# Kernel optimization log

Measured on AMD Instinct MI355X. Metric: run time of the kernel, lower is better.

## Reference

```python
import jax, jax.numpy as jnp
import numpy as np
import math

D_MODEL = 1024
D_STATE = 64
D_CONV = 4
EXPAND = 2
D_INNER = EXPAND * D_MODEL
DT_RANK = max(16, D_MODEL // 16)
SEQ_LEN = 2048
BATCH = 4

def setup_inputs() -> dict:
    key = jax.random.key(0)
    ks = jax.random.split(key, 16)
    s = lambda *sh: 1.0 / math.sqrt(sh[-1])
    x = jax.random.normal(ks[0], (SEQ_LEN, BATCH, D_MODEL), jnp.float32)
    state = jnp.zeros((BATCH, D_INNER, D_STATE), jnp.float32)
    W_in = jax.random.normal(ks[1], (2 * D_INNER, D_MODEL), jnp.float32) * s(2 * D_INNER, D_MODEL)
    b_in = jnp.zeros((2 * D_INNER,), jnp.float32)
    conv_w = jax.random.normal(ks[2], (D_INNER, 1, D_CONV), jnp.float32) * s(1, D_CONV)
    conv_b = jnp.zeros((D_INNER,), jnp.float32)
    W_xp = jax.random.normal(ks[3], (DT_RANK + 2 * D_STATE, D_INNER), jnp.float32) * s(1, D_INNER)
    b_xp = jnp.zeros((DT_RANK + 2 * D_STATE,), jnp.float32)
    W_dt = jax.random.normal(ks[4], (D_INNER, DT_RANK), jnp.float32) * s(1, DT_RANK)
    # dt bias init as in module: softplus-inverse of dt in [1e-3, 0.1]
    dt = jnp.exp(jax.random.uniform(ks[5], (D_INNER,)) * (math.log(0.1) - math.log(0.001)) + math.log(0.001))
    b_dt = dt + jnp.log(-jnp.expm1(-dt))
    A_log = jnp.log(jnp.broadcast_to(jnp.arange(1, D_STATE + 1, dtype=jnp.float32)[None, :], (D_INNER, D_STATE)))
    D = jnp.ones((D_INNER,), jnp.float32)
    W_out = jax.random.normal(ks[6], (D_MODEL, D_INNER), jnp.float32) * s(1, D_INNER)
    b_out = jnp.zeros((D_MODEL,), jnp.float32)
    ln_g = jnp.ones((D_MODEL,), jnp.float32)
    ln_b = jnp.zeros((D_MODEL,), jnp.float32)
    return dict(x=x, state=state, W_in=W_in, b_in=b_in, conv_w=conv_w, conv_b=conv_b,
                W_xp=W_xp, b_xp=b_xp, W_dt=W_dt, b_dt=b_dt, A_log=A_log, D=D,
                W_out=W_out, b_out=b_out, ln_g=ln_g, ln_b=ln_b)

def _silu(v):
    return v * jax.nn.sigmoid(v)

def _forward(x, state, W_in, b_in, conv_w, conv_b, W_xp, b_xp, W_dt, b_dt, A_log, D, W_out, b_out, ln_g, ln_b):
    S, B, _ = x.shape
    xz = x @ W_in.T + b_in                      # [S,B,2*di]
    x_inner, z = jnp.split(xz, 2, axis=-1)      # [S,B,di] each
    # causal depthwise conv1d: pad left (d_conv-1), matching conv1d(pad=K-1)[..., :S]
    xc = jnp.transpose(x_inner, (1, 2, 0))      # [B,di,S]
    xc = jax.lax.conv_general_dilated(
        xc, conv_w, window_strides=(1,), padding=[(D_CONV - 1, 0)],
        dimension_numbers=('NCH', 'OIH', 'NCH'), feature_group_count=D_INNER)
    xc = xc + conv_b[None, :, None]
    x_conv = _silu(jnp.transpose(xc, (2, 0, 1)))  # [S,B,di]
    # input-dependent projections over full sequence
    xp = x_conv @ W_xp.T + b_xp                 # [S,B,dt_rank+2*ds]
    dt_low, B_seq, C_seq = jnp.split(xp, [DT_RANK, DT_RANK + D_STATE], axis=-1)
    # NOTE: original adds dt_proj.bias twice (Linear already includes it)
    dt = jax.nn.softplus(dt_low @ W_dt.T + 2.0 * b_dt)  # [S,B,di]
    A = -jnp.exp(A_log)                         # [di,ds]

    def step(carry, inp):
        dt_t, B_t, C_t, x_t = inp               # [B,di],[B,ds],[B,ds],[B,di]
        dA = jnp.exp(dt_t[..., None] * A)       # [B,di,ds]
        dBx = (dt_t * x_t)[..., None] * B_t[:, None, :]  # [B,di,ds]
        new = carry * dA + dBx
        y = jnp.einsum('bdn,bn->bd', new, C_t) + D * x_t
        return new, y

    final_state, ys = jax.lax.scan(step, state, (dt, B_seq, C_seq, x_conv))
    ys = ys * _silu(z)                          # [S,B,di]
    out = jnp.mean(ys, axis=0) @ W_out.T + b_out  # [B,d_model]
    mu = jnp.mean(out, axis=-1, keepdims=True)
    var = jnp.var(out, axis=-1, keepdims=True)
    out = (out - mu) / jnp.sqrt(var + 1e-5) * ln_g + ln_b
    return out, final_state

def reference(x, state, W_in, b_in, conv_w, conv_b, W_xp, b_xp, W_dt, b_dt, A_log, D, W_out, b_out, ln_g, ln_b):
    return _forward(x, state, W_in, b_in, conv_w, conv_b, W_xp, b_xp, W_dt, b_dt, A_log, D, W_out, b_out, ln_g, ln_b)
```

## Files before the change

### kernel.cpp

```cpp
#include <hip/hip_runtime.h>
#include <hip/hip_fp16.h>

typedef __attribute__((ext_vector_type(8))) short short8;
typedef __attribute__((ext_vector_type(8))) unsigned short u16x8;
typedef __attribute__((ext_vector_type(4))) float f32x4;

#define S_LEN 2048
#define BATCH 4
#define DM 1024
#define DI 2048
#define DS 64
#define DTR 64
#define XPW 192
#define NCH 16
#define CLEN 128

typedef const __attribute__((address_space(4))) unsigned* cu_as4;

__device__ __forceinline__ unsigned short f2bf(float f){
  unsigned u = __builtin_bit_cast(unsigned, f);
  u += 0x7fffu + ((u >> 16) & 1u);
  return (unsigned short)(u >> 16);
}
__device__ __forceinline__ float bf2f(unsigned short h){
  unsigned u = ((unsigned)h) << 16;
  return __builtin_bit_cast(float, u);
}
__device__ __forceinline__ void gload16(const void* g, void* l){
  __builtin_amdgcn_global_load_lds((const __attribute__((address_space(1))) void*)g,
                                   (__attribute__((address_space(3))) void*)l, 16, 0, 0);
}
__device__ __forceinline__ float siluf_(float v){ return v / (1.f + __expf(-v)); }

__global__ __launch_bounds__(256) void cvt_all_k(const float* __restrict__ i0, unsigned short* __restrict__ o0,
                                                 const float* __restrict__ i1, unsigned short* __restrict__ o1,
                                                 const float* __restrict__ i2, unsigned short* __restrict__ o2,
                                                 const float* __restrict__ i3, unsigned short* __restrict__ o3)
{
  int bid = blockIdx.x;
  const float* in; unsigned short* out; int base;
  if (bid < 8192)       { in = i0; out = o0; base = bid; }
  else if (bid < 12288) { in = i1; out = o1; base = bid - 8192; }
  else if (bid < 12672) { in = i2; out = o2; base = bid - 12288; }
  else                  { in = i3; out = o3; base = bid - 12672; }
  int i = (base * 256 + threadIdx.x) * 4;
  float4 v = *(const float4*)(in + i);
  ushort4 o;
  o.x = f2bf(v.x); o.y = f2bf(v.y); o.z = f2bf(v.z); o.w = f2bf(v.w);
  *(ushort4*)(out + i) = o;
}

template<int EPI>
__global__ __launch_bounds__(256)
void gemm_bt(const unsigned short* __restrict__ A, const unsigned short* __restrict__ B,
             const float* __restrict__ bias,
             int N, int K, int lda, int ldb,
             void* __restrict__ vp0, void* __restrict__ vp1,
             const void* __restrict__ vp2, const void* __restrict__ vp3,
             int nsilu, float* __restrict__ sdt)
{
  __shared__ unsigned short As[128 * 32];
  __shared__ unsigned short Bs[128 * 32];
  const int tid  = threadIdx.x;
  const int lane = tid & 63;
  const int wid  = tid >> 6;
  int bm, bn;
  if constexpr (EPI == 2) {
    int flat = blockIdx.y * 64 + blockIdx.x;
    int swz = (flat & 7) * 256 + (flat >> 3);
    bm = swz & 63; bn = swz >> 6;
  } else {
    bm = blockIdx.x; bn = blockIdx.y;
  }
  int k_lo = 0, k_hi = K;
  if constexpr (EPI == 3) { k_lo = blockIdx.z * 512; k_hi = k_lo + 512; }
  const int r0 = tid >> 2;
  const int c0 = (tid & 3) * 8;
  int brow0 = bn * 128 + r0;        if (brow0 > N - 1) brow0 = N - 1;
  int brow1 = bn * 128 + 64 + r0;   if (brow1 > N - 1) brow1 = N - 1;
  const unsigned short* pa0 = A + (size_t)(bm * 128 + r0) * lda + c0;
  const unsigned short* pa1 = A + (size_t)(bm * 128 + 64 + r0) * lda + c0;
  const unsigned short* pb0 = B + (size_t)brow0 * ldb + c0;
  const unsigned short* pb1 = B + (size_t)brow1 * ldb + c0;
  f32x4 acc[4][4] = {};
  const int fr = lane & 15, fq = lane >> 4;
  const int wm = (wid >> 1) * 64, wn = (wid & 1) * 64;
  const int aoff0 = (wm + fr) * 32 + fq * 8;
  const int boff0 = (wn + fr) * 32 + fq * 8;
  for (int k0 = k_lo; k0 < k_hi; k0 += 32) {
    __syncthreads();
    gload16(pa0 + k0, &As[tid * 8]);
    gload16(pa1 + k0, &As[2048 + tid * 8]);
    gload16(pb0 + k0, &Bs[tid * 8]);
    gload16(pb1 + k0, &Bs[2048 + tid * 8]);
    __syncthreads();
    short8 av[4], bv[4];
#pragma unroll
    for (int i = 0; i < 4; i++) av[i] = *(const short8*)&As[aoff0 + i * 16 * 32];
#pragma unroll
    for (int i = 0; i < 4; i++) bv[i] = *(const short8*)&Bs[boff0 + i * 16 * 32];
#pragma unroll
    for (int i = 0; i < 4; i++)
#pragma unroll
      for (int j = 0; j < 4; j++)
        acc[i][j] = __builtin_amdgcn_mfma_f32_16x16x32_bf16(av[i], bv[j], acc[i][j], 0, 0, 0);
  }

  if constexpr (EPI == 3) {
    float* xpp = (float*)vp0;
    const size_t kb = (size_t)blockIdx.z * 8192 * 256;
#pragma unroll
    for (int i = 0; i < 4; i++) {
#pragma unroll
      for (int j = 0; j < 4; j++) {
        int gc = bn * 128 + wn + j * 16 + fr;
#pragma unroll
        for (int e = 0; e < 4; e++) {
          int gr = bm * 128 + wm + i * 16 + fq * 4 + e;
          xpp[kb + (size_t)gr * 256 + gc] = acc[i][j][e];
        }
      }
    }
  } else if constexpr (EPI == 2) {
    unsigned short* xib = (unsigned short*)vp0;
    unsigned short* grm = (unsigned short*)vp1;
#pragma unroll
    for (int i = 0; i < 4; i++) {
#pragma unroll
      for (int j = 0; j < 4; j++) {
        int gc = bn * 128 + wn + j * 16 + fr;
        float bb = bias[gc];
#pragma unroll
        for (int e = 0; e < 4; e++) {
          int gr = bm * 128 + wm + i * 16 + fq * 4 + e;
          float v = acc[i][j][e] + bb;
          if (gc < nsilu) xib[(size_t)gr * DI + gc] = f2bf(v);
          else            grm[(size_t)gr * DI + (gc - nsilu)] = f2bf(siluf_(v));
        }
      }
    }
  } else {
    unsigned* dtH = (unsigned*)vp0;
    unsigned* dxg = (unsigned*)vp1;
    const unsigned short* xcb = (const unsigned short*)vp2;
    const unsigned short* grm = (const unsigned short*)vp3;
#pragma unroll
    for (int j = 0; j < 4; j++) {
      int gc = bn * 128 + wn + j * 16 + fr;
      float bb2 = 2.f * bias[gc];
#pragma unroll
      for (int i = 0; i < 4; i++)
#pragma unroll
        for (int e = 0; e < 4; e++) {
          float v = acc[i][j][e] + bb2;
          acc[i][j][e] = fmaxf(v, 0.f) + log1pf(__expf(-fabsf(v)));
        }
    }
    __shared__ unsigned short hbuf[256 * 36];
    const int myc = wn >> 6;
    const int tbase = wm / 4;
    const int chk = bm >> 2;
    for (int cc = 0; cc < 2; ++cc) {
      __syncthreads();
      if (myc == cc) {
#pragma unroll
        for (int i = 0; i < 4; i++)
#pragma unroll
          for (int j = 0; j < 4; j++) {
            int dl = j * 16 + fr;
            int t_ = tbase + i * 4 + fq;
#pragma unroll
            for (int e = 0; e < 4; e++)
              hbuf[(e * 64 + dl) * 36 + t_] = f2bf(acc[i][j][e]);
          }
      }
      __syncthreads();
#pragma unroll
      for (int k = 0; k < 4; ++k) {
        int gidx = tid + k * 256;
        int t   = gidx & 31;
        int gl8 = (gidx >> 5) & 7;
        int e   = gidx >> 8;
        int R   = e * 64 + gl8 * 8;
        uint4 o;
        o.x = (unsigned)hbuf[(R+0)*36 + t] | ((unsigned)hbuf[(R+1)*36 + t] << 16);
        o.y = (unsigned)hbuf[(R+2)*36 + t] | ((unsigned)hbuf[(R+3)*36 + t] << 16);
        o.z = (unsigned)hbuf[(R+4)*36 + t] | ((unsigned)hbuf[(R+5)*36 + t] << 16);
        o.w = (unsigned)hbuf[(R+6)*36 + t] | ((unsigned)hbuf[(R+7)*36 + t] << 16);
        size_t G = (size_t)(bn * 16 + cc * 8 + gl8);
        *(uint4*)&dtH[(((size_t)e * 256 + G) * 2048 + bm * 32 + t) * 4] = o;
      }
#pragma unroll
      for (int k = 0; k < 4; ++k) {
        int gidx = tid + k * 256;
        int t   = gidx & 31;
        int gl8 = (gidx >> 5) & 7;
        int e   = gidx >> 8;
        int gr  = (bm * 32 + t) * 4 + e;
        int col = bn * 128 + cc * 64 + gl8 * 8;
        u16x8 xv = *(const u16x8*)&xcb[(size_t)gr * DI + col];
        u16x8 gv = *(const u16x8*)&grm[(size_t)gr * DI + col];
        int R = e * 64 + gl8 * 8;
        unsigned ow[8];
#pragma unroll
        for (int u = 0; u < 8; ++u) {
          float dt = bf2f(hbuf[(R + u) * 36 + t]);
          float dtx = dt * bf2f((unsigned short)xv[u]);
          ow[u] = ((unsigned)f2bf(dtx) << 16) | (unsigned)(unsigned short)gv[u];
        }
        size_t G = (size_t)(bn * 16 + cc * 8 + gl8);
        unsigned* dst = &dxg[(((size_t)e * 256 + G) * 2048 + bm * 32 + t) * 8];
        uint4 o0, o1;
        o0.x = ow[0]; o0.y = ow[1]; o0.z = ow[2]; o0.w = ow[3];
        o1.x = ow[4]; o1.y = ow[5]; o1.z = ow[6]; o1.w = ow[7];
        *(uint4*)dst = o0;
        *(uint4*)(dst + 4) = o1;
      }
      {
        int e  = tid >> 6;
        int dl = tid & 63;
        float s = 0.f;
#pragma unroll
        for (int t = 0; t < 32; ++t)
          s += bf2f(hbuf[(e * 64 + dl) * 36 + t]);
        int g8 = bn * 16 + cc * 8 + (dl >> 3);
        atomicAdd(&sdt[(((size_t)e * NCH + chk) * 256 + g8) * 8 + (dl & 7)], s);
      }
    }
  }
}

__global__ __launch_bounds__(192) void xpred_k(const float* __restrict__ xpp,
                                               const float* __restrict__ bias,
                                               unsigned short* __restrict__ xpb,
                                               float* __restrict__ bcI)
{
  const int gr = blockIdx.x;
  const int gc = threadIdx.x;
  const size_t o = (size_t)gr * 256 + gc;
  float v = xpp[o] + xpp[o + 2097152] + xpp[o + 2 * 2097152] + xpp[o + 3 * 2097152] + bias[gc];
  xpb[(size_t)gr * XPW + gc] = f2bf(v);
  if (gc >= 64 && gc < 128)      bcI[((size_t)gr * 64 + gc - 64) * 2 + 0] = v;
  else if (gc >= 128)            bcI[((size_t)gr * 64 + gc - 128) * 2 + 1] = v;
}

__global__ __launch_bounds__(256) void convsxg_k(const unsigned short* __restrict__ xib,
                                                 const unsigned short* __restrict__ grm,
                                                 const float* __restrict__ cw,
                                                 const float* __restrict__ cb,
                                                 unsigned short* __restrict__ xcb,
                                                 float* __restrict__ sxg)
{
  const int d4 = blockIdx.x * 1024 + threadIdx.x * 4;
  const int b  = blockIdx.y;
  const int t0 = blockIdx.z * 16;
  float4 cwv[4]; float cbv[4];
#pragma unroll
  for (int j = 0; j < 4; ++j) { cwv[j] = *(const float4*)&cw[(d4 + j) * 4]; cbv[j] = cb[d4 + j]; }
  ushort4 z4; z4.x = z4.y = z4.z = z4.w = 0;
  ushort4 xm1 = (t0 >= 1) ? *(const ushort4*)&xib[((size_t)((t0 - 1) * 4 + b)) * DI + d4] : z4;
  ushort4 xm2 = (t0 >= 2) ? *(const ushort4*)&xib[((size_t)((t0 - 2) * 4 + b)) * DI + d4] : z4;
  ushort4 xm3 = (t0 >= 3) ? *(const ushort4*)&xib[((size_t)((t0 - 3) * 4 + b)) * DI + d4] : z4;
  float sa[4] = {0.f, 0.f, 0.f, 0.f};
  for (int tt = 0; tt < 16; ++tt) {
    const int t = t0 + tt;
    const size_t row = ((size_t)(t * 4 + b)) * DI + d4;
    ushort4 x0 = *(const ushort4*)&xib[row];
    ushort4 gv = *(const ushort4*)&grm[row];
    unsigned short xr[4] = {x0.x, x0.y, x0.z, x0.w};
    unsigned short r1[4] = {xm1.x, xm1.y, xm1.z, xm1.w};
    unsigned short r2[4] = {xm2.x, xm2.y, xm2.z, xm2.w};
    unsigned short r3[4] = {xm3.x, xm3.y, xm3.z, xm3.w};
    unsigned short gg[4] = {gv.x, gv.y, gv.z, gv.w};
    unsigned short ov[4];
#pragma unroll
    for (int j = 0; j < 4; ++j) {
      float s = cbv[j];
      s = fmaf(cwv[j].w, bf2f(xr[j]), s);
      s = fmaf(cwv[j].z, bf2f(r1[j]), s);
      s = fmaf(cwv[j].y, bf2f(r2[j]), s);
      s = fmaf(cwv[j].x, bf2f(r3[j]), s);
      ov[j] = f2bf(siluf_(s));
      sa[j] = fmaf(bf2f(ov[j]), bf2f(gg[j]), sa[j]);
    }
    ushort4 o; o.x = ov[0]; o.y = ov[1]; o.z = ov[2]; o.w = ov[3];
    *(ushort4*)&xcb[row] = o;
    xm3 = xm2; xm2 = xm1; xm1 = x0;
  }
#pragma unroll
  for (int j = 0; j < 4; ++j) atomicAdd(&sxg[b * DI + d4 + j], sa[j]);
}

__global__ __launch_bounds__(256) void scan_k(const unsigned* __restrict__ dtHg,
                                              const unsigned* __restrict__ dxgg,
                                              const float* __restrict__ bcI,
                                              const float* __restrict__ A_log,
                                              float* __restrict__ Pb,
                                              float* __restrict__ Fb,
                                              float* __restrict__ accp)
{
  const int tid  = threadIdx.x;
  const int lane = tid & 63;
  const int gw = __builtin_amdgcn_readfirstlane(blockIdx.x * 4 + (tid >> 6));
  const int b  = gw >> 12;
  const int c  = (gw >> 8) & 15;
  const int g  = gw & 255;
  const int d0 = g * 8;
  const float LOG2E = 1.4426950408889634f;
  float a2[8], st[8], Dr[8], Fr[8], acc[8];
#pragma unroll
  for (int j = 0; j < 8; ++j) {
    a2[j] = -__expf(A_log[(size_t)(d0 + j) * DS + lane]) * LOG2E;
    st[j] = 0.f; Dr[j] = 1.f; Fr[j] = 0.f; acc[j] = 0.f;
  }
  cu_as4 pdt = (cu_as4)(unsigned long long)(dtHg + (((size_t)(b * 256 + g)) * S_LEN + c * CLEN) * 4);
  cu_as4 pdx = (cu_as4)(unsigned long long)(dxgg + (((size_t)(b * 256 + g)) * S_LEN + c * CLEN) * 8);
  const float* pbc = bcI + (((size_t)(c * CLEN) * 4 + b) * 64 + lane) * 2;
#pragma unroll 4
  for (int t = 0; t < CLEN; ++t) {
    unsigned dw0 = pdt[t * 4 + 0], dw1 = pdt[t * 4 + 1];
    unsigned dw2 = pdt[t * 4 + 2], dw3 = pdt[t * 4 + 3];
    unsigned xs[8];
#pragma unroll
    for (int j = 0; j < 8; ++j) xs[j] = pdx[t * 8 + j];
    float2 bc = *(const float2*)(pbc + (size_t)t * 512);
    float dts[8];
    dts[0] = __builtin_bit_cast(float, dw0 << 16);
    dts[1] = __builtin_bit_cast(float, dw0 & 0xffff0000u);
    dts[2] = __builtin_bit_cast(float, dw1 << 16);
    dts[3] = __builtin_bit_cast(float, dw1 & 0xffff0000u);
    dts[4] = __builtin_bit_cast(float, dw2 << 16);
    dts[5] = __builtin_bit_cast(float, dw2 & 0xffff0000u);
    dts[6] = __builtin_bit_cast(float, dw3 << 16);
    dts[7] = __builtin_bit_cast(float, dw3 & 0xffff0000u);
#pragma unroll
    for (int j = 0; j < 8; ++j) {
      float dxs = __builtin_bit_cast(float, xs[j] & 0xffff0000u);
      float gsv = __builtin_bit_cast(float, xs[j] << 16);
      float dA = __builtin_amdgcn_exp2f(dts[j] * a2[j]);
      st[j] = fmaf(st[j], dA, dxs * bc.x);
      Dr[j] *= dA;
      float w = gsv * bc.y;
      acc[j] = fmaf(st[j], w, acc[j]);
      Fr[j] = fmaf(Dr[j], w, Fr[j]);
    }
  }
  const size_t sb = (((size_t)((b * NCH + c) * 256 + g)) * 8) * 64 + lane;
#pragma unroll
  for (int j = 0; j < 8; ++j) {
    Pb[sb + j * 64] = st[j];
    Fb[sb + j * 64] = Fr[j];
  }
#pragma unroll
  for (int j = 0; j < 8; ++j)
#pragma unroll
    for (int m = 32; m; m >>= 1) acc[j] += __shfl_xor(acc[j], m, 64);
  if (lane == 0) {
#pragma unroll
    for (int j = 0; j < 8; ++j)
      accp[(b * NCH + c) * DI + d0 + j] = acc[j];
  }
}

__global__ __launch_bounds__(256) void fixup_k(const float* __restrict__ Pb,
                                               const float* __restrict__ Fb,
                                               const float* __restrict__ sdt,
                                               const float* __restrict__ accp,
                                               const float* __restrict__ A_log,
                                               const float* __restrict__ state_in,
                                               float* __restrict__ accbuf,
                                               float* __restrict__ state_out)
{
  const int tid  = threadIdx.x;
  const int lane = tid & 63;
  const int gw = blockIdx.x * 4 + (tid >> 6);
  const int b  = gw >> 8;
  const int g  = gw & 255;
  const int d0 = g * 8;
  const float LOG2E = 1.4426950408889634f;
  float a2[8], S[8], v[8];
#pragma unroll
  for (int j = 0; j < 8; ++j) {
    a2[j] = -__expf(A_log[(size_t)(d0 + j) * DS + lane]) * LOG2E;
    S[j] = state_in[((size_t)(b * DI + d0 + j)) * DS + lane];
    v[j] = 0.f;
  }
#pragma unroll
  for (int c = 0; c < NCH; ++c) {
    const size_t sb = (((size_t)((b * NCH + c) * 256 + g)) * 8) * 64 + lane;
    const size_t se = (((size_t)(b * NCH + c)) * 256 + g) * 8;
#pragma unroll
    for (int j = 0; j < 8; ++j) {
      float P = Pb[sb + j * 64], F = Fb[sb + j * 64];
      float E = __builtin_amdgcn_exp2f(a2[j] * sdt[se + j]);
      v[j] = fmaf(F, S[j], v[j]);
      S[j] = fmaf(E, S[j], P);
    }
  }
#pragma unroll
  for (int j = 0; j < 8; ++j)
    state_out[((size_t)(b * DI + d0 + j)) * DS + lane] = S[j];
#pragma unroll
  for (int j = 0; j < 8; ++j)
#pragma unroll
    for (int m = 32; m; m >>= 1) v[j] += __shfl_xor(v[j], m, 64);
  if (lane == 0) {
#pragma unroll
    for (int j = 0; j < 8; ++j) {
      float s = v[j];
#pragma unroll
      for (int c = 0; c < NCH; ++c) s += accp[(b * NCH + c) * DI + d0 + j];
      accbuf[b * DI + d0 + j] = s;
    }
  }
}

__global__ __launch_bounds__(256) void out_gemm_k(const float* __restrict__ accb,
                                                  const float* __restrict__ sxg,
                                                  const float* __restrict__ Dv,
                                                  const float* __restrict__ W_out,
                                                  const float* __restrict__ b_out,
                                                  float* __restrict__ outpre)
{
  int b = blockIdx.y;
  int m = blockIdx.x * 8 + (threadIdx.x >> 5);
  int dl = threadIdx.x & 31;
  const float* wr = W_out + (size_t)m * DI;
  const float* ac = accb + b * DI;
  const float* sx = sxg + b * DI;
  float p = 0.f;
  for (int dd = dl; dd < DI; dd += 32) {
    float av = fmaf(Dv[dd], sx[dd], ac[dd]);
    p = fmaf(wr[dd], av, p);
  }
#pragma unroll
  for (int s = 16; s; s >>= 1) p += __shfl_xor(p, s, 32);
  if (dl == 0) outpre[b * DM + m] = p * (1.f / 2048.f) + b_out[m];
}

__global__ __launch_bounds__(256) void ln_k(const float* __restrict__ outpre,
                                            const float* __restrict__ g,
                                            const float* __restrict__ bta,
                                            float* __restrict__ dout)
{
  int b = blockIdx.x;
  const float* row = outpre + b * DM;
  float s = 0.f, s2 = 0.f, vv[4];
#pragma unroll
  for (int i = 0; i < 4; i++) {
    float v = row[threadIdx.x + i * 256];
    vv[i] = v; s += v; s2 += v * v;
  }
#pragma unroll
  for (int m = 32; m; m >>= 1) { s += __shfl_xor(s, m, 64); s2 += __shfl_xor(s2, m, 64); }
  __shared__ float rs[4], rs2[4];
  int w = threadIdx.x >> 6;
  if ((threadIdx.x & 63) == 0) { rs[w] = s; rs2[w] = s2; }
  __syncthreads();
  float S = rs[0] + rs[1] + rs[2] + rs[3];
  float S2 = rs2[0] + rs2[1] + rs2[2] + rs2[3];
  float mu = S * (1.f / 1024.f);
  float var = S2 * (1.f / 1024.f) - mu * mu;
  float inv = rsqrtf(var + 1e-5f);
#pragma unroll
  for (int i = 0; i < 4; i++) {
    int c = threadIdx.x + i * 256;
    dout[b * DM + c] = (vv[i] - mu) * inv * g[c] + bta[c];
  }
}

extern "C" void kernel_launch(void* const* d_in, const int* in_sizes, int n_in,
                              void* d_out, int out_size, void* d_ws, size_t ws_size,
                              hipStream_t stream)
{
  const float* x      = (const float*)d_in[0];
  const float* state0 = (const float*)d_in[1];
  const float* W_in   = (const float*)d_in[2];
  const float* b_in   = (const float*)d_in[3];
  const float* conv_w = (const float*)d_in[4];
  const float* conv_b = (const float*)d_in[5];
  const float* W_xp   = (const float*)d_in[6];
  const float* b_xp   = (const float*)d_in[7];
  const float* W_dt   = (const float*)d_in[8];
  const float* b_dt   = (const float*)d_in[9];
  const float* A_log  = (const float*)d_in[10];
  const float* Dvec   = (const float*)d_in[11];
  const float* W_out  = (const float*)d_in[12];
  const float* b_out  = (const float*)d_in[13];
  const float* ln_g   = (const float*)d_in[14];
  const float* ln_b   = (const float*)d_in[15];
  float* out = (float*)d_out;

  const size_t MB = 1024 * 1024;
  char* ws = (char*)d_ws;
  unsigned short* grm  = (unsigned short*)(ws + 0);
  unsigned short* xcb  = (unsigned short*)(ws + 32  * MB);
  unsigned short* xib  = (unsigned short*)(ws + 64  * MB);
  unsigned*       dtH  = (unsigned*)(ws + 64  * MB);
  unsigned short* xb   = (unsigned short*)(ws + 96  * MB);
  unsigned short* wbin = (unsigned short*)(ws + 112 * MB);
  float*          xpp  = (float*)(ws + 96 * MB);
  unsigned*       dxg  = (unsigned*)(ws + 96  * MB);
  unsigned short* xpb  = (unsigned short*)(ws + 160 * MB);
  float*          bcI  = (float*)(ws + 163 * MB);
  unsigned short* wbxp = (unsigned short*)(ws + 167 * MB);
  unsigned short* wbdt = (unsigned short*)(ws + 167 * MB + 786432);
  float*          sxg    = (float*)(ws + 168 * MB);
  float*          sdt    = (float*)(ws + 168 * MB + 32768);
  float*          accb   = (float*)(ws + 168 * MB + 557056);
  float*          outpre = (float*)(ws + 168 * MB + 589824);
  float*          accp   = (float*)(ws + 168 * MB + 606208);
  float*          Pb   = (float*)(ws + 0);
  float*          Fb   = (float*)(ws + 32 * MB);

  cvt_all_k<<<12800, 256, 0, stream>>>(x, xb, W_in, wbin, W_xp, wbxp, W_dt, wbdt);
  hipMemsetAsync(sxg, 0, 557056, stream);
  gemm_bt<2><<<dim3(64, 32), 256, 0, stream>>>(xb, wbin, b_in, 4096, 1024, 1024, 1024,
                                               xib, grm, nullptr, nullptr, 2048, nullptr);
  convsxg_k<<<dim3(2, 4, 128), 256, 0, stream>>>(xib, grm, conv_w, conv_b, xcb, sxg);
  gemm_bt<3><<<dim3(64, 2, 4), 256, 0, stream>>>(xcb, wbxp, nullptr, 192, 2048, 2048, 2048,
                                                 xpp, nullptr, nullptr, nullptr, 0, nullptr);
  xpred_k<<<8192, 192, 0, stream>>>(xpp, b_xp, xpb, bcI);
  gemm_bt<1><<<dim3(64, 16), 256, 0, stream>>>(xpb, wbdt, b_dt, 2048, 64, XPW, 64,
                                               dtH, dxg, xcb, grm, 0, sdt);
  scan_k<<<4096, 256, 0, stream>>>(dtH, dxg, bcI, A_log, Pb, Fb, accp);
  fixup_k<<<256, 256, 0, stream>>>(Pb, Fb, sdt, accp, A_log, state0, accb, out + 4096);
  out_gemm_k<<<dim3(128, 4), 256, 0, stream>>>(accb, sxg, Dvec, W_out, b_out, outpre);
  ln_k<<<4, 256, 0, stream>>>(outpre, ln_g, ln_b, out);
}
```

Measured before the change: 487.3 us.

## Add dedicated multi-stage pipelined input-projection GEMM kernel

Replaces the generic gemm_bt<2> input projection with a specialized kernel that keeps four LDS stages and issues global-to-LDS loads three tiles ahead, using explicit vmcnt waits and one barrier per k-step. It also uses a swizzled LDS layout for bank-conflict avoidance, splits MFMA groups with interleaved loads, and raises wave priority around MFMAs. This hides global load latency in the largest GEMM, at the cost of 64KB of LDS per block, which lowers occupancy.

```diff
diff --git a/kernel.cpp b/kernel.cpp
--- a/kernel.cpp
+++ b/kernel.cpp
@@ -50,6 +50,105 @@
   *(ushort4*)(out + i) = o;
 }
 
+__global__ __launch_bounds__(256)
+void gemm_in8_k(const unsigned short* __restrict__ A, const unsigned short* __restrict__ B,
+                const float* __restrict__ bias,
+                unsigned short* __restrict__ xib, unsigned short* __restrict__ grm)
+{
+  __shared__ unsigned short As[4][4096];
+  __shared__ unsigned short Bs[4][4096];
+  const int tid  = threadIdx.x;
+  const int lane = tid & 63;
+  const int wid  = tid >> 6;
+  int flat = blockIdx.y * 64 + blockIdx.x;
+  int swz = (flat & 7) * 256 + (flat >> 3);
+  const int bm = swz & 63, bn = swz >> 6;
+
+  const unsigned short* srcA[2]; const unsigned short* srcB[2];
+  int ldso[2];
+#pragma unroll
+  for (int q = 0; q < 2; ++q) {
+    int s   = q * 256 + tid;
+    int row = ((s >> 5) << 3) | (s & 7);
+    int seg = (s >> 3) & 3;
+    srcA[q] = A + (size_t)(bm * 128 + row) * 1024 + seg * 8;
+    srcB[q] = B + (size_t)(bn * 128 + row) * 1024 + seg * 8;
+    ldso[q] = s * 8;
+  }
+  const int fr = lane & 15, fq = lane >> 4;
+  const int wm = (wid >> 1) * 64, wn = (wid & 1) * 64;
+  int aoff[4], boff[4];
+#pragma unroll
+  for (int f = 0; f < 4; ++f) {
+    aoff[f] = ((((wm >> 3) + 2 * f + (fr >> 3)) * 32) + fq * 8 + (fr & 7)) * 8;
+    boff[f] = ((((wn >> 3) + 2 * f + (fr >> 3)) * 32) + fq * 8 + (fr & 7)) * 8;
+  }
+
+#define GLA(t,q) gload16(srcA[q] + (size_t)(t) * 32, &As[(t) & 3][ldso[q]])
+#define GLB(t,q) gload16(srcB[q] + (size_t)(t) * 32, &Bs[(t) & 3][ldso[q]])
+#pragma unroll
+  for (int t = 0; t < 3; ++t) { GLA(t,0); GLA(t,1); GLB(t,0); GLB(t,1); }
+  asm volatile("s_waitcnt vmcnt(8)" ::: "memory");
+  __builtin_amdgcn_sched_barrier(0);
+  __builtin_amdgcn_s_barrier();
+  __builtin_amdgcn_sched_barrier(0);
+
+  f32x4 acc[4][4] = {};
+  for (int kt = 0; kt < 32; ++kt) {
+    const int buf = kt & 3;
+    if (kt + 3 < 32) { GLA(kt + 3, 0); GLA(kt + 3, 1); }
+    short8 bv[4];
+#pragma unroll
+    for (int j = 0; j < 4; ++j) bv[j] = *(const short8*)&Bs[buf][boff[j]];
+    short8 av0 = *(const short8*)&As[buf][aoff[0]];
+    short8 av1 = *(const short8*)&As[buf][aoff[1]];
+    __builtin_amdgcn_s_setprio(1);
+#pragma unroll
+    for (int j = 0; j < 4; ++j)
+      acc[0][j] = __builtin_amdgcn_mfma_f32_16x16x32_bf16(av0, bv[j], acc[0][j], 0, 0, 0);
+#pragma unroll
+    for (int j = 0; j < 4; ++j)
+      acc[1][j] = __builtin_amdgcn_mfma_f32_16x16x32_bf16(av1, bv[j], acc[1][j], 0, 0, 0);
+    __builtin_amdgcn_s_setprio(0);
+    if (kt + 3 < 32) { GLB(kt + 3, 0); GLB(kt + 3, 1); }
+    short8 av2 = *(const short8*)&As[buf][aoff[2]];
+    short8 av3 = *(const short8*)&As[buf][aoff[3]];
+    __builtin_amdgcn_s_setprio(1);
+#pragma unroll
+    for (int j = 0; j < 4; ++j)
+      acc[2][j] = __builtin_amdgcn_mfma_f32_16x16x32_bf16(av2, bv[j], acc[2][j], 0, 0, 0);
+#pragma unroll
+    for (int j = 0; j < 4; ++j)
+      acc[3][j] = __builtin_amdgcn_mfma_f32_16x16x32_bf16(av3, bv[j], acc[3][j], 0, 0, 0);
+    __builtin_amdgcn_s_setprio(0);
+    if (kt == 31) break;
+    if (kt <= 28)      asm volatile("s_waitcnt vmcnt(8)" ::: "memory");
+    else if (kt == 29) asm volatile("s_waitcnt vmcnt(4)" ::: "memory");
+    else               asm volatile("s_waitcnt vmcnt(0)" ::: "memory");
+    __builtin_amdgcn_sched_barrier(0);
+    __builtin_amdgcn_s_barrier();
+    __builtin_amdgcn_sched_barrier(0);
+  }
+#undef GLA
+#undef GLB
+
+#pragma unroll
+  for (int i = 0; i < 4; i++) {
+#pragma unroll
+    for (int j = 0; j < 4; j++) {
+      int gc = bn * 128 + wn + j * 16 + fr;
+      float bb = bias[gc];
+#pragma unroll
+      for (int e = 0; e < 4; e++) {
+        int gr = bm * 128 + wm + i * 16 + fq * 4 + e;
+        float v = acc[i][j][e] + bb;
+        if (gc < 2048) xib[(size_t)gr * DI + gc] = f2bf(v);
+        else           grm[(size_t)gr * DI + (gc - 2048)] = f2bf(siluf_(v));
+      }
+    }
+  }
+}
+
 template<int EPI>
 __global__ __launch_bounds__(256)
 void gemm_bt(const unsigned short* __restrict__ A, const unsigned short* __restrict__ B,
@@ -64,14 +163,7 @@
   const int tid  = threadIdx.x;
   const int lane = tid & 63;
   const int wid  = tid >> 6;
-  int bm, bn;
-  if constexpr (EPI == 2) {
-    int flat = blockIdx.y * 64 + blockIdx.x;
-    int swz = (flat & 7) * 256 + (flat >> 3);
-    bm = swz & 63; bn = swz >> 6;
-  } else {
-    bm = blockIdx.x; bn = blockIdx.y;
-  }
+  int bm = blockIdx.x, bn = blockIdx.y;
   int k_lo = 0, k_hi = K;
   if constexpr (EPI == 3) { k_lo = blockIdx.z * 512; k_hi = k_lo + 512; }
   const int r0 = tid >> 2;
@@ -121,24 +213,6 @@
         }
       }
     }
-  } else if constexpr (EPI == 2) {
-    unsigned short* xib = (unsigned short*)vp0;
-    unsigned short* grm = (unsigned short*)vp1;
-#pragma unroll
-    for (int i = 0; i < 4; i++) {
-#pragma unroll
-      for (int j = 0; j < 4; j++) {
-        int gc = bn * 128 + wn + j * 16 + fr;
-        float bb = bias[gc];
-#pragma unroll
-        for (int e = 0; e < 4; e++) {
-          int gr = bm * 128 + wm + i * 16 + fq * 4 + e;
-          float v = acc[i][j][e] + bb;
-          if (gc < nsilu) xib[(size_t)gr * DI + gc] = f2bf(v);
-          else            grm[(size_t)gr * DI + (gc - nsilu)] = f2bf(siluf_(v));
-        }
-      }
-    }
   } else {
     unsigned* dtH = (unsigned*)vp0;
     unsigned* dxg = (unsigned*)vp1;
@@ -515,8 +589,7 @@
 
   cvt_all_k<<<12800, 256, 0, stream>>>(x, xb, W_in, wbin, W_xp, wbxp, W_dt, wbdt);
   hipMemsetAsync(sxg, 0, 557056, stream);
-  gemm_bt<2><<<dim3(64, 32), 256, 0, stream>>>(xb, wbin, b_in, 4096, 1024, 1024, 1024,
-                                               xib, grm, nullptr, nullptr, 2048, nullptr);
+  gemm_in8_k<<<dim3(64, 32), 256, 0, stream>>>(xb, wbin, b_in, xib, grm);
   convsxg_k<<<dim3(2, 4, 128), 256, 0, stream>>>(xib, grm, conv_w, conv_b, xcb, sxg);
   gemm_bt<3><<<dim3(64, 2, 4), 256, 0, stream>>>(xcb, wbxp, nullptr, 192, 2048, 2048, 2048,
                                                  xpp, nullptr, nullptr, nullptr, 0, nullptr);
```

Result: slower. 537.9 us (+10.4%).
